# Kernel optimization log

Measured on AMD Instinct MI355X. Metric: run time of the kernel, lower is better.

## Reference

```python
import jax, jax.numpy as jnp
import numpy as np

D_MODEL = 1024
N_HEADS = 16
HEAD_DIM = D_MODEL // N_HEADS


def setup_inputs() -> dict:
    key = jax.random.key(0)
    ks = jax.random.split(key, 9)
    s = 1.0 / np.sqrt(D_MODEL)
    x = jax.random.normal(ks[0], (2, 2048, D_MODEL), dtype=jnp.float32)
    Wq = jax.random.uniform(ks[1], (D_MODEL, D_MODEL), jnp.float32, -s, s)
    bq = jax.random.uniform(ks[2], (D_MODEL,), jnp.float32, -s, s)
    Wk = jax.random.uniform(ks[3], (D_MODEL, D_MODEL), jnp.float32, -s, s)
    bk = jax.random.uniform(ks[4], (D_MODEL,), jnp.float32, -s, s)
    Wv = jax.random.uniform(ks[5], (D_MODEL, D_MODEL), jnp.float32, -s, s)
    bv = jax.random.uniform(ks[6], (D_MODEL,), jnp.float32, -s, s)
    Wo = jax.random.uniform(ks[7], (D_MODEL, D_MODEL), jnp.float32, -s, s)
    bo = jax.random.uniform(ks[8], (D_MODEL,), jnp.float32, -s, s)
    return {"x": x, "Wq": Wq, "bq": bq, "Wk": Wk, "bk": bk,
            "Wv": Wv, "bv": bv, "Wo": Wo, "bo": bo}


def reference(x, Wq, bq, Wk, bk, Wv, bv, Wo, bo):
    B, L, _ = x.shape
    # Linear projections (torch Linear: y = x @ W.T + b; here W stored as [in, out])
    def split_heads(t):  # [B, L, D] -> [B, H, L, hd]
        return t.reshape(B, L, N_HEADS, HEAD_DIM).transpose(0, 2, 1, 3)
    Q = split_heads(x @ Wq + bq)
    K = split_heads(x @ Wk + bk)
    V = split_heads(x @ Wv + bv)
    scores = jnp.einsum('bhqd,bhkd->bhqk', Q, K) / np.sqrt(HEAD_DIM).astype(np.float32)
    attn = jax.nn.softmax(scores, axis=-1)
    out = jnp.einsum('bhqk,bhkd->bhqd', attn, V)
    out = out.transpose(0, 2, 1, 3).reshape(B, L, D_MODEL)
    return out @ Wo + bo
```

## Files before the change

### kernel.cpp

```cpp
#include <hip/hip_runtime.h>

typedef float f32x4  __attribute__((ext_vector_type(4)));
typedef short s16x8  __attribute__((ext_vector_type(8)));
typedef short s16x4  __attribute__((ext_vector_type(4)));
typedef unsigned short u16x8 __attribute__((ext_vector_type(8)));
typedef unsigned int   u32x2 __attribute__((ext_vector_type(2)));
typedef unsigned int   u32x4 __attribute__((ext_vector_type(4)));

#define DM   1024
#define LSEQ 2048
#define NH   16
#define HD   64
#define MTOT 4096
#define RS   3072

__device__ __forceinline__ unsigned short f2bf(float f) {
  union { float f; unsigned int u; } v; v.f = f;
  unsigned int r = (v.u + 0x7fffu + ((v.u >> 16) & 1u)) >> 16;
  return (unsigned short)r;
}

__device__ __forceinline__ unsigned cvtpk(float lo, float hi) {
  unsigned r;
  asm volatile("v_cvt_pk_bf16_f32 %0, %1, %2" : "=v"(r) : "v"(lo), "v"(hi));
  return r;
}
__device__ __forceinline__ s16x8 cvt8(float4 a, float4 b) {
  u32x4 o = {cvtpk(a.x, a.y), cvtpk(a.z, a.w), cvtpk(b.x, b.y), cvtpk(b.z, b.w)};
  return __builtin_bit_cast(s16x8, o);
}

__global__ __launch_bounds__(256) void wtrans4(const float* __restrict__ W0,
                                               const float* __restrict__ W1,
                                               const float* __restrict__ W2,
                                               const float* __restrict__ W3,
                                               unsigned short* __restrict__ Wt) {
  __shared__ __align__(16) unsigned short t[64][72];
  const int z = blockIdx.z;
  const float* W = (z == 0) ? W0 : (z == 1) ? W1 : (z == 2) ? W2 : W3;
  unsigned short* dst = Wt + (size_t)z * DM * DM;
  const int n0 = blockIdx.x * 64, k0 = blockIdx.y * 64;
  const int r = threadIdx.x >> 4, c4 = (threadIdx.x & 15) * 4;
#pragma unroll
  for (int rr = r; rr < 64; rr += 16) {
    float4 v = *(const float4*)&W[(long)(k0 + rr) * DM + n0 + c4];
    ushort4 u;
    u.x = f2bf(v.x); u.y = f2bf(v.y); u.z = f2bf(v.z); u.w = f2bf(v.w);
    *(ushort4*)&t[rr][c4] = u;
  }
  __syncthreads();
#pragma unroll
  for (int rr = r; rr < 64; rr += 16) {
    ushort4 u;
    u.x = t[c4 + 0][rr]; u.y = t[c4 + 1][rr];
    u.z = t[c4 + 2][rr]; u.w = t[c4 + 3][rr];
    *(ushort4*)&dst[(long)(n0 + rr) * DM + k0 + c4] = u;
  }
}

template <int QKV_MODE>
__global__ __launch_bounds__(256) void gemm_bt(
    const void* __restrict__ Aptr, const unsigned short* __restrict__ Bt,
    const float* __restrict__ bias0, const float* __restrict__ bias1,
    const float* __restrict__ bias2, void* __restrict__ Cout,
    unsigned short* __restrict__ VT, int N, int K) {
  __shared__ __align__(16) unsigned short As[128][72];
  __shared__ __align__(16) unsigned short Bs[128][72];
  const int tid = threadIdx.x;
  const int lane = tid & 63, w = tid >> 6;
  const int r16 = lane & 15, g = lane >> 4;
  const int m0 = blockIdx.y * 128, n0 = blockIdx.x * 128;
  const int wm = (w >> 1) * 64, wn = (w & 1) * 64;
  const int srow = tid >> 2, scol = (tid & 3) * 8;
  const float* Agf = (const float*)Aptr + (long)(m0 + srow) * K + scol;
  const unsigned short* Agh = (const unsigned short*)Aptr + (long)(m0 + srow) * K + scol;
  const unsigned short* Bg = Bt + (long)(n0 + srow) * K + scol;
  f32x4 acc[4][4] = {};
  float4 fa0, fa1, fa2, fa3, fa4, fa5, fa6, fa7;
  s16x8 a0, a1, a2, a3, b0, b1, b2, b3;

#define GLOAD_AB(koff)                                                        \
  {                                                                           \
    if constexpr (QKV_MODE) {                                                 \
      const float* p = Agf + (koff);                                          \
      fa0 = *(const float4*)p;        fa1 = *(const float4*)(p + 4);          \
      fa2 = *(const float4*)(p + 32); fa3 = *(const float4*)(p + 36);         \
      const float* q = p + 64L * K;                                           \
      fa4 = *(const float4*)q;        fa5 = *(const float4*)(q + 4);          \
      fa6 = *(const float4*)(q + 32); fa7 = *(const float4*)(q + 36);         \
    } else {                                                                  \
      const unsigned short* p = Agh + (koff);                                 \
      a0 = *(const s16x8*)p;             a1 = *(const s16x8*)(p + 32);        \
      a2 = *(const s16x8*)(p + 64L * K); a3 = *(const s16x8*)(p + 64L * K + 32); \
    }                                                                         \
    const unsigned short* pb = Bg + (koff);                                   \
    b0 = *(const s16x8*)pb;             b1 = *(const s16x8*)(pb + 32);        \
    b2 = *(const s16x8*)(pb + 64L * K); b3 = *(const s16x8*)(pb + 64L * K + 32); \
  }

  GLOAD_AB(0);
  for (int kt = 0; kt < K; kt += 64) {
    __syncthreads();
    if constexpr (QKV_MODE) {
      *(s16x8*)&As[srow][scol]           = cvt8(fa0, fa1);
      *(s16x8*)&As[srow][scol + 32]      = cvt8(fa2, fa3);
      *(s16x8*)&As[srow + 64][scol]      = cvt8(fa4, fa5);
      *(s16x8*)&As[srow + 64][scol + 32] = cvt8(fa6, fa7);
    } else {
      *(s16x8*)&As[srow][scol]           = a0;
      *(s16x8*)&As[srow][scol + 32]      = a1;
      *(s16x8*)&As[srow + 64][scol]      = a2;
      *(s16x8*)&As[srow + 64][scol + 32] = a3;
    }
    *(s16x8*)&Bs[srow][scol]           = b0;
    *(s16x8*)&Bs[srow][scol + 32]      = b1;
    *(s16x8*)&Bs[srow + 64][scol]      = b2;
    *(s16x8*)&Bs[srow + 64][scol + 32] = b3;
    __syncthreads();
    if (kt + 64 < K) GLOAD_AB(kt + 64);
#pragma unroll
    for (int kk = 0; kk < 64; kk += 32) {
      s16x8 af[4], bf[4];
#pragma unroll
      for (int i = 0; i < 4; i++) af[i] = *(const s16x8*)&As[wm + i * 16 + r16][kk + g * 8];
#pragma unroll
      for (int j = 0; j < 4; j++) bf[j] = *(const s16x8*)&Bs[wn + j * 16 + r16][kk + g * 8];
#pragma unroll
      for (int i = 0; i < 4; i++)
#pragma unroll
        for (int j = 0; j < 4; j++)
          acc[i][j] = __builtin_amdgcn_mfma_f32_16x16x32_bf16(af[i], bf[j], acc[i][j], 0, 0, 0);
    }
  }
#undef GLOAD_AB

  if (QKV_MODE && n0 >= 2048) {
#pragma unroll
    for (int i = 0; i < 4; i++) {
      const int row0 = m0 + wm + i * 16 + g * 4;
      const int b = row0 >> 11, seq = row0 & 2047;
#pragma unroll
      for (int j = 0; j < 4; j++) {
        const int cv = n0 + wn + j * 16 + r16 - 2048;
        const float bb = bias2[cv];
        const int bh = b * NH + (cv >> 6), d = cv & 63;
        ushort4 u;
        u.x = f2bf(acc[i][j][0] + bb);
        u.y = f2bf(acc[i][j][1] + bb);
        u.z = f2bf(acc[i][j][2] + bb);
        u.w = f2bf(acc[i][j][3] + bb);
        *(ushort4*)(VT + ((size_t)bh * HD + d) * LSEQ + seq) = u;
      }
    }
    return;
  }
#pragma unroll
  for (int i = 0; i < 4; i++) {
#pragma unroll
    for (int j = 0; j < 4; j++) {
      const int row = m0 + wm + i * 16 + g * 4;
      const int col = n0 + wn + j * 16 + r16;
      float bb, sc = 1.0f;
      if constexpr (QKV_MODE) {
        bb = (col < 1024) ? bias0[col] : bias1[col - 1024];
        if (col < 1024) sc = 0.18033688011112042f;
      } else {
        bb = bias0[col];
      }
#pragma unroll
      for (int r = 0; r < 4; r++) {
        float v = (acc[i][j][r] + bb) * sc;
        if constexpr (QKV_MODE)
          ((unsigned short*)Cout)[(long)(row + r) * N + col] = f2bf(v);
        else
          ((float*)Cout)[(long)(row + r) * N + col] = v;
      }
    }
  }
}

__global__ __launch_bounds__(512) void attn9(const unsigned short* __restrict__ QKV,
                                             const unsigned short* __restrict__ VT,
                                             unsigned short* __restrict__ O) {
  __shared__ __align__(16) unsigned short Ks[2][2][64][76];
  __shared__ __align__(16) unsigned short Vs[2][2][64][76];
  __shared__ float Lsum[4][32];
  const int tid = threadIdx.x;
  const int lane = tid & 63, w = tid >> 6;
  const int wq = w & 3;
  const int hb = tid >> 8;
  const int r16 = lane & 15, g = lane >> 4;
  const int qb = blockIdx.x, bh = blockIdx.y;
  const int b = bh >> 4, h = bh & 15;

  const unsigned short* QgA =
      QKV + (size_t)(b * LSEQ + qb * 128 + wq * 32 + r16) * RS + h * HD;
  const unsigned short* QgB = QgA + 16 * RS;
  const s16x8 qa0 = *(const s16x8*)&QgA[g * 8];
  const s16x8 qa1 = *(const s16x8*)&QgA[32 + g * 8];
  const s16x8 qb0 = *(const s16x8*)&QgB[g * 8];
  const s16x8 qb1 = *(const s16x8*)&QgB[32 + g * 8];

  const unsigned short* Kb =
      QKV + (size_t)(b * LSEQ + hb * 1024) * RS + DM + h * HD;
  const unsigned short* Vb =
      VT + (size_t)(bh * HD) * LSEQ + hb * 1024;
  const int t256 = tid & 255;
  const int srow = t256 >> 2, scol = (t256 & 3) * 8;

  f32x4 oA[4] = {}, oB[4] = {};
  float psA[4] = {0.f, 0.f, 0.f, 0.f};
  float psB[4] = {0.f, 0.f, 0.f, 0.f};

  s16x8 k0 = *(const s16x8*)&Kb[(size_t)srow * RS + scol];
  s16x8 k1 = *(const s16x8*)&Kb[(size_t)srow * RS + scol + 32];
  s16x8 v0 = *(const s16x8*)&Vb[(size_t)srow * LSEQ + scol];
  s16x8 v1 = *(const s16x8*)&Vb[(size_t)srow * LSEQ + scol + 32];
  *(s16x8*)&Ks[hb][0][srow][scol]      = k0;
  *(s16x8*)&Ks[hb][0][srow][scol + 32] = k1;
  *(s16x8*)&Vs[hb][0][srow][scol]      = v0;
  *(s16x8*)&Vs[hb][0][srow][scol + 32] = v1;
  __syncthreads();

  for (int tt = 0; tt < 16; ++tt) {
    const int cur = tt & 1;
    if (tt + 1 < 16) {
      const size_t ko = (size_t)((tt + 1) * 64 + srow) * RS + scol;
      const size_t vo = (size_t)srow * LSEQ + (tt + 1) * 64 + scol;
      k0 = *(const s16x8*)&Kb[ko];
      k1 = *(const s16x8*)&Kb[ko + 32];
      v0 = *(const s16x8*)&Vb[vo];
      v1 = *(const s16x8*)&Vb[vo + 32];
    }

    f32x4 sA[4], sB[4];
#pragma unroll
    for (int kc = 0; kc < 4; kc++) {
      s16x8 kb0 = *(const s16x8*)&Ks[hb][cur][kc * 16 + r16][g * 8];
      s16x8 kb1 = *(const s16x8*)&Ks[hb][cur][kc * 16 + r16][32 + g * 8];
      f32x4 zA = {}, zB = {};
      zA = __builtin_amdgcn_mfma_f32_16x16x32_bf16(kb0, qa0, zA, 0, 0, 0);
      sA[kc] = __builtin_amdgcn_mfma_f32_16x16x32_bf16(kb1, qa1, zA, 0, 0, 0);
      zB = __builtin_amdgcn_mfma_f32_16x16x32_bf16(kb0, qb0, zB, 0, 0, 0);
      sB[kc] = __builtin_amdgcn_mfma_f32_16x16x32_bf16(kb1, qb1, zB, 0, 0, 0);
    }

    s16x4 paA[4], paB[4];
#pragma unroll
    for (int kc = 0; kc < 4; kc++) {
      float a0f = exp2f(sA[kc][0]);
      float a1f = exp2f(sA[kc][1]);
      float a2f = exp2f(sA[kc][2]);
      float a3f = exp2f(sA[kc][3]);
      psA[0] += a0f; psA[1] += a1f; psA[2] += a2f; psA[3] += a3f;
      u32x2 pkA = {cvtpk(a0f, a1f), cvtpk(a2f, a3f)};
      paA[kc] = __builtin_bit_cast(s16x4, pkA);
      float b0f = exp2f(sB[kc][0]);
      float b1f = exp2f(sB[kc][1]);
      float b2f = exp2f(sB[kc][2]);
      float b3f = exp2f(sB[kc][3]);
      psB[0] += b0f; psB[1] += b1f; psB[2] += b2f; psB[3] += b3f;
      u32x2 pkB = {cvtpk(b0f, b1f), cvtpk(b2f, b3f)};
      paB[kc] = __builtin_bit_cast(s16x4, pkB);
    }

#pragma unroll
    for (int kc = 0; kc < 4; kc++)
#pragma unroll
      for (int dc = 0; dc < 4; dc++) {
        s16x4 vb = *(const s16x4*)&Vs[hb][cur][dc * 16 + r16][kc * 16 + 4 * g];
        oA[dc] = __builtin_amdgcn_mfma_f32_16x16x16bf16_1k(paA[kc], vb, oA[dc], 0, 0, 0);
        oB[dc] = __builtin_amdgcn_mfma_f32_16x16x16bf16_1k(paB[kc], vb, oB[dc], 0, 0, 0);
      }

    if (tt + 1 < 16) {
      *(s16x8*)&Ks[hb][cur ^ 1][srow][scol]      = k0;
      *(s16x8*)&Ks[hb][cur ^ 1][srow][scol + 32] = k1;
      *(s16x8*)&Vs[hb][cur ^ 1][srow][scol]      = v0;
      *(s16x8*)&Vs[hb][cur ^ 1][srow][scol + 32] = v1;
      __syncthreads();
    }
  }

  __syncthreads();
  float (*xo)[33] = reinterpret_cast<float(*)[33]>(&Ks[0][0][0][0]);
  float (*xs)[9]  = reinterpret_cast<float(*)[9]>(&Vs[0][0][0][0]);
  if (w >= 4) {
    const int l = tid & 255;
#pragma unroll
    for (int dc = 0; dc < 4; dc++) {
      *(f32x4*)&xo[l][4 * dc]      = oA[dc];
      *(f32x4*)&xo[l][16 + 4 * dc] = oB[dc];
    }
#pragma unroll
    for (int r = 0; r < 4; r++) { xs[l][r] = psA[r]; xs[l][4 + r] = psB[r]; }
  }
  __syncthreads();
  float totA = 0.f, totB = 0.f;
  if (w < 4) {
    const int l = tid;
#pragma unroll
    for (int dc = 0; dc < 4; dc++) {
      oA[dc] += *(const f32x4*)&xo[l][4 * dc];
      oB[dc] += *(const f32x4*)&xo[l][16 + 4 * dc];
    }
#pragma unroll
    for (int r = 0; r < 4; r++) { psA[r] += xs[l][r]; psB[r] += xs[l][4 + r]; }
    totA = psA[0] + psA[1] + psA[2] + psA[3];
    totA += __shfl_xor(totA, 16);
    totA += __shfl_xor(totA, 32);
    totB = psB[0] + psB[1] + psB[2] + psB[3];
    totB += __shfl_xor(totB, 16);
    totB += __shfl_xor(totB, 32);
    if (g == 0) {
      Lsum[wq][r16]      = totA;
      Lsum[wq][16 + r16] = totB;
    }
  }
  __syncthreads();
  if (w < 4) {
    const float4 svA = *(const float4*)&Lsum[wq][4 * g];
    const float4 svB = *(const float4*)&Lsum[wq][16 + 4 * g];
    unsigned short* Og = O + (size_t)(b * LSEQ + qb * 128 + wq * 32) * DM + h * HD;
#pragma unroll
    for (int r = 0; r < 4; r++) {
      const float invA = 1.0f / ((const float*)&svA)[r];
      const float invB = 1.0f / ((const float*)&svB)[r];
#pragma unroll
      for (int dc = 0; dc < 4; dc++) {
        Og[(size_t)(g * 4 + r) * DM + dc * 16 + r16]      = f2bf(oA[dc][r] * invA);
        Og[(size_t)(16 + g * 4 + r) * DM + dc * 16 + r16] = f2bf(oB[dc][r] * invB);
      }
    }
  }
}

extern "C" void kernel_launch(void* const* d_in, const int* in_sizes, int n_in,
                              void* d_out, int out_size, void* d_ws, size_t ws_size,
                              hipStream_t stream) {
  const float* x  = (const float*)d_in[0];
  const float* Wq = (const float*)d_in[1];
  const float* bq = (const float*)d_in[2];
  const float* Wk = (const float*)d_in[3];
  const float* bk = (const float*)d_in[4];
  const float* Wv = (const float*)d_in[5];
  const float* bv = (const float*)d_in[6];
  const float* Wo = (const float*)d_in[7];
  const float* bo = (const float*)d_in[8];

  unsigned short* VTb  = (unsigned short*)d_ws;
  unsigned short* Wcat = VTb + (size_t)MTOT * DM;
  unsigned short* Wot  = Wcat + (size_t)3 * DM * DM;
  unsigned short* QKVb = Wot + (size_t)DM * DM;
  unsigned short* Ob   = QKVb + (size_t)MTOT * 3 * DM;

  wtrans4<<<dim3(16, 16, 4), 256, 0, stream>>>(Wq, Wk, Wv, Wo, Wcat);

  gemm_bt<1><<<dim3(3 * DM / 128, MTOT / 128), 256, 0, stream>>>(
      (const void*)x, Wcat, bq, bk, bv, (void*)QKVb, VTb, 3 * DM, DM);
  attn9<<<dim3(LSEQ / 128, 2 * NH), 512, 0, stream>>>(QKVb, VTb, Ob);
  gemm_bt<0><<<dim3(DM / 128, MTOT / 128), 256, 0, stream>>>(
      (const void*)Ob, Wot, bo, nullptr, nullptr, d_out, nullptr, DM, DM);
}
```

Measured before the change: 137.2 us.

## Software-pipeline attention with triple-buffered K/V and next-tile QK overlap

Changes the attention kernel to triple-buffer the K/V tiles in shared memory and compute QK scores for the next tile before the exp/PV work on the current one. Global loads now run two tiles ahead. The goal is to overlap score MFMAs with the softmax ALU work and to hide global load latency. In exchange it uses more LDS and registers (extra score arrays), which could lower occupancy or cause spills.

```diff
diff --git a/kernel.cpp b/kernel.cpp
--- a/kernel.cpp
+++ b/kernel.cpp
@@ -179,11 +179,11 @@
   }
 }
 
-__global__ __launch_bounds__(512) void attn9(const unsigned short* __restrict__ QKV,
-                                             const unsigned short* __restrict__ VT,
-                                             unsigned short* __restrict__ O) {
-  __shared__ __align__(16) unsigned short Ks[2][2][64][76];
-  __shared__ __align__(16) unsigned short Vs[2][2][64][76];
+__global__ __launch_bounds__(512) void attn11(const unsigned short* __restrict__ QKV,
+                                              const unsigned short* __restrict__ VT,
+                                              unsigned short* __restrict__ O) {
+  __shared__ __align__(16) unsigned short Ks[2][3][64][76];
+  __shared__ __align__(16) unsigned short Vs[2][3][64][76];
   __shared__ float Lsum[4][32];
   const int tid = threadIdx.x;
   const int lane = tid & 63, w = tid >> 6;
@@ -212,53 +212,64 @@
   float psA[4] = {0.f, 0.f, 0.f, 0.f};
   float psB[4] = {0.f, 0.f, 0.f, 0.f};
 
-  s16x8 k0 = *(const s16x8*)&Kb[(size_t)srow * RS + scol];
-  s16x8 k1 = *(const s16x8*)&Kb[(size_t)srow * RS + scol + 32];
-  s16x8 v0 = *(const s16x8*)&Vb[(size_t)srow * LSEQ + scol];
-  s16x8 v1 = *(const s16x8*)&Vb[(size_t)srow * LSEQ + scol + 32];
-  *(s16x8*)&Ks[hb][0][srow][scol]      = k0;
-  *(s16x8*)&Ks[hb][0][srow][scol + 32] = k1;
-  *(s16x8*)&Vs[hb][0][srow][scol]      = v0;
-  *(s16x8*)&Vs[hb][0][srow][scol + 32] = v1;
-  __syncthreads();
-
+#define LOAD_TILE(tt)                                                     \
+  {                                                                       \
+    const size_t ko = (size_t)((tt) * 64 + srow) * RS + scol;             \
+    const size_t vo = (size_t)srow * LSEQ + (tt) * 64 + scol;             \
+    k0 = *(const s16x8*)&Kb[ko];                                          \
+    k1 = *(const s16x8*)&Kb[ko + 32];                                     \
+    v0 = *(const s16x8*)&Vb[vo];                                          \
+    v1 = *(const s16x8*)&Vb[vo + 32];                                     \
+  }
+#define WRITE_TILE(buf)                                                   \
+  {                                                                       \
+    *(s16x8*)&Ks[hb][buf][srow][scol]      = k0;                          \
+    *(s16x8*)&Ks[hb][buf][srow][scol + 32] = k1;                          \
+    *(s16x8*)&Vs[hb][buf][srow][scol]      = v0;                          \
+    *(s16x8*)&Vs[hb][buf][srow][scol + 32] = v1;                          \
+  }
+#define QK_TILE(buf, sA, sB)                                              \
+  _Pragma("unroll")                                                       \
+  for (int kc = 0; kc < 4; kc++) {                                        \
+    s16x8 kb0 = *(const s16x8*)&Ks[hb][buf][kc * 16 + r16][g * 8];        \
+    s16x8 kb1 = *(const s16x8*)&Ks[hb][buf][kc * 16 + r16][32 + g * 8];   \
+    f32x4 zA = {}, zB = {};                                               \
+    zA = __builtin_amdgcn_mfma_f32_16x16x32_bf16(kb0, qa0, zA, 0, 0, 0);  \
+    sA[kc] = __builtin_amdgcn_mfma_f32_16x16x32_bf16(kb1, qa1, zA, 0, 0, 0); \
+    zB = __builtin_amdgcn_mfma_f32_16x16x32_bf16(kb0, qb0, zB, 0, 0, 0);  \
+    sB[kc] = __builtin_amdgcn_mfma_f32_16x16x32_bf16(kb1, qb1, zB, 0, 0, 0); \
+  }
+
+  s16x8 k0, k1, v0, v1;
+  f32x4 spA[4], spB[4], snA[4], snB[4];
+
+  LOAD_TILE(0);
+  WRITE_TILE(0);
+  LOAD_TILE(1);
+  __syncthreads();
+  QK_TILE(0, spA, spB);
+  WRITE_TILE(1);
+  LOAD_TILE(2);
+  __syncthreads();
+
+  int cur = 0, nxt = 1, wrt = 2;
   for (int tt = 0; tt < 16; ++tt) {
-    const int cur = tt & 1;
-    if (tt + 1 < 16) {
-      const size_t ko = (size_t)((tt + 1) * 64 + srow) * RS + scol;
-      const size_t vo = (size_t)srow * LSEQ + (tt + 1) * 64 + scol;
-      k0 = *(const s16x8*)&Kb[ko];
-      k1 = *(const s16x8*)&Kb[ko + 32];
-      v0 = *(const s16x8*)&Vb[vo];
-      v1 = *(const s16x8*)&Vb[vo + 32];
-    }
-
-    f32x4 sA[4], sB[4];
+    if (tt + 1 < 16) QK_TILE(nxt, snA, snB);
+
+    s16x4 paA[4], paB[4];
 #pragma unroll
     for (int kc = 0; kc < 4; kc++) {
-      s16x8 kb0 = *(const s16x8*)&Ks[hb][cur][kc * 16 + r16][g * 8];
-      s16x8 kb1 = *(const s16x8*)&Ks[hb][cur][kc * 16 + r16][32 + g * 8];
-      f32x4 zA = {}, zB = {};
-      zA = __builtin_amdgcn_mfma_f32_16x16x32_bf16(kb0, qa0, zA, 0, 0, 0);
-      sA[kc] = __builtin_amdgcn_mfma_f32_16x16x32_bf16(kb1, qa1, zA, 0, 0, 0);
-      zB = __builtin_amdgcn_mfma_f32_16x16x32_bf16(kb0, qb0, zB, 0, 0, 0);
-      sB[kc] = __builtin_amdgcn_mfma_f32_16x16x32_bf16(kb1, qb1, zB, 0, 0, 0);
-    }
-
-    s16x4 paA[4], paB[4];
-#pragma unroll
-    for (int kc = 0; kc < 4; kc++) {
-      float a0f = exp2f(sA[kc][0]);
-      float a1f = exp2f(sA[kc][1]);
-      float a2f = exp2f(sA[kc][2]);
-      float a3f = exp2f(sA[kc][3]);
+      float a0f = exp2f(spA[kc][0]);
+      float a1f = exp2f(spA[kc][1]);
+      float a2f = exp2f(spA[kc][2]);
+      float a3f = exp2f(spA[kc][3]);
       psA[0] += a0f; psA[1] += a1f; psA[2] += a2f; psA[3] += a3f;
       u32x2 pkA = {cvtpk(a0f, a1f), cvtpk(a2f, a3f)};
       paA[kc] = __builtin_bit_cast(s16x4, pkA);
-      float b0f = exp2f(sB[kc][0]);
-      float b1f = exp2f(sB[kc][1]);
-      float b2f = exp2f(sB[kc][2]);
-      float b3f = exp2f(sB[kc][3]);
+      float b0f = exp2f(spB[kc][0]);
+      float b1f = exp2f(spB[kc][1]);
+      float b2f = exp2f(spB[kc][2]);
+      float b3f = exp2f(spB[kc][3]);
       psB[0] += b0f; psB[1] += b1f; psB[2] += b2f; psB[3] += b3f;
       u32x2 pkB = {cvtpk(b0f, b1f), cvtpk(b2f, b3f)};
       paB[kc] = __builtin_bit_cast(s16x4, pkB);
@@ -273,14 +284,21 @@
         oB[dc] = __builtin_amdgcn_mfma_f32_16x16x16bf16_1k(paB[kc], vb, oB[dc], 0, 0, 0);
       }
 
+    if (tt + 2 < 16) {
+      WRITE_TILE(wrt);
+      if (tt + 3 < 16) LOAD_TILE(tt + 3);
+    }
+
     if (tt + 1 < 16) {
-      *(s16x8*)&Ks[hb][cur ^ 1][srow][scol]      = k0;
-      *(s16x8*)&Ks[hb][cur ^ 1][srow][scol + 32] = k1;
-      *(s16x8*)&Vs[hb][cur ^ 1][srow][scol]      = v0;
-      *(s16x8*)&Vs[hb][cur ^ 1][srow][scol + 32] = v1;
       __syncthreads();
-    }
-  }
+#pragma unroll
+      for (int kc = 0; kc < 4; kc++) { spA[kc] = snA[kc]; spB[kc] = snB[kc]; }
+      int t = cur; cur = nxt; nxt = wrt; wrt = t;
+    }
+  }
+#undef LOAD_TILE
+#undef WRITE_TILE
+#undef QK_TILE
 
   __syncthreads();
   float (*xo)[33] = reinterpret_cast<float(*)[33]>(&Ks[0][0][0][0]);
@@ -358,7 +376,7 @@
 
   gemm_bt<1><<<dim3(3 * DM / 128, MTOT / 128), 256, 0, stream>>>(
       (const void*)x, Wcat, bq, bk, bv, (void*)QKVb, VTb, 3 * DM, DM);
-  attn9<<<dim3(LSEQ / 128, 2 * NH), 512, 0, stream>>>(QKVb, VTb, Ob);
+  attn11<<<dim3(LSEQ / 128, 2 * NH), 512, 0, stream>>>(QKVb, VTb, Ob);
   gemm_bt<0><<<dim3(DM / 128, MTOT / 128), 256, 0, stream>>>(
       (const void*)Ob, Wot, bo, nullptr, nullptr, d_out, nullptr, DM, DM);
 }
```

New measurement: 140.0 us. About the same (+2.0%).
